# Optimization experiments

Measured on AMD Instinct MI355X. Metric: run time of the kernel, lower is better.

Reference implementation:

```python
import jax, jax.numpy as jnp
import numpy as np

N_NODES = 50000
N_EDGES = 640000
D_IN = 128
D_H1 = 128
D_H2 = 128
N_CLASSES = 64


def setup_inputs() -> dict:
    key = jax.random.key(0)
    ks = jax.random.split(key, 8)
    x = jax.random.normal(ks[0], (N_NODES, D_IN), dtype=jnp.float32)
    edge_index = jax.random.randint(ks[1], (2, N_EDGES), 0, N_NODES, dtype=jnp.int64)
    s1 = 1.0 / np.sqrt(D_IN)
    s2 = 1.0 / np.sqrt(D_H1)
    s3 = 1.0 / np.sqrt(D_H2)
    W1 = jax.random.uniform(ks[2], (D_IN, D_H1), jnp.float32, -s1, s1)
    b1 = jnp.zeros((D_H1,), jnp.float32)
    W2 = jax.random.uniform(ks[3], (D_H1, D_H2), jnp.float32, -s2, s2)
    b2 = jnp.zeros((D_H2,), jnp.float32)
    Wl = jax.random.uniform(ks[4], (D_H2, N_CLASSES), jnp.float32, -s3, s3)
    bl = jax.random.uniform(ks[5], (N_CLASSES,), jnp.float32, -s3, s3)
    return {"x": x, "edge_index": edge_index, "W1": W1, "b1": b1,
            "W2": W2, "b2": b2, "Wl": Wl, "bl": bl}


def _gcn_norm(edge_index, num_nodes):
    # PyG GCNConv: add self-loops, symmetric normalization D^-1/2 (A+I) D^-1/2
    loop = jnp.arange(num_nodes, dtype=edge_index.dtype)
    src = jnp.concatenate([edge_index[0], loop])
    dst = jnp.concatenate([edge_index[1], loop])
    deg = jax.ops.segment_sum(jnp.ones_like(dst, dtype=jnp.float32), dst,
                              num_segments=num_nodes)
    dinv = jnp.where(deg > 0, jax.lax.rsqrt(deg), 0.0)
    norm = dinv[src] * dinv[dst]  # [E+N]
    return src, dst, norm


def _gcn_conv(h, src, dst, norm, W, b, num_nodes):
    h = h @ W                       # transform first (smaller gather when D_out small)
    msg = h[src] * norm[:, None]    # gather + per-edge scale  [E+N, D_out]
    agg = jax.ops.segment_sum(msg, dst, num_segments=num_nodes)  # scatter-add
    return agg + b


def reference(x, edge_index, W1, b1, W2, b2, Wl, bl):
    n = x.shape[0]
    src, dst, norm = _gcn_norm(edge_index, n)
    h = jax.nn.relu(_gcn_conv(x, src, dst, norm, W1, b1, n))
    # dropout is identity in eval mode
    h = jax.nn.relu(_gcn_conv(h, src, dst, norm, W2, b2, n))
    return h @ Wl + bl
```

## Files before the change

kernel.cpp:

```cpp
#include <hip/hip_runtime.h>


typedef __attribute__((ext_vector_type(8))) __bf16 bf16x8;
typedef __attribute__((ext_vector_type(8))) short short8;
typedef __attribute__((ext_vector_type(4))) float f32x4;

__device__ inline float bf_lo(unsigned u) { return __uint_as_float(u << 16); }
__device__ inline float bf_hi(unsigned u) { return __uint_as_float(u & 0xffff0000u); }
__device__ inline unsigned short f2bf(float v) {
  return __builtin_bit_cast(unsigned short, (__bf16)v);
}

__global__ void k_count(const int* __restrict__ dst, int E, int* __restrict__ cnt) {
  int i = blockIdx.x * blockDim.x + threadIdx.x;
  if (i < E) atomicAdd(&cnt[dst[i]], 1);
}

__global__ void k_scan1(const int* __restrict__ cnt, int n, int* __restrict__ partial) {
  __shared__ int s[256];
  int i = blockIdx.x * 256 + threadIdx.x;
  s[threadIdx.x] = (i < n) ? cnt[i] : 0;
  __syncthreads();
  for (int off = 128; off > 0; off >>= 1) {
    if (threadIdx.x < off) s[threadIdx.x] += s[threadIdx.x + off];
    __syncthreads();
  }
  if (threadIdx.x == 0) partial[blockIdx.x] = s[0];
}

__global__ void k_scan2(int* __restrict__ partial, int nb) {
  __shared__ int s[256];
  int t = threadIdx.x;
  int v = (t < nb) ? partial[t] : 0;
  s[t] = v;
  __syncthreads();
  for (int off = 1; off < 256; off <<= 1) {
    int u = (t >= off) ? s[t - off] : 0;
    __syncthreads();
    s[t] += u;
    __syncthreads();
  }
  if (t < nb) partial[t] = s[t] - v;
}

__global__ void k_scan3(const int* __restrict__ cnt, const int* __restrict__ partial,
                        int n, int* __restrict__ row_off, int* __restrict__ cursor,
                        float* __restrict__ dinv) {
  __shared__ int s[256];
  int t = threadIdx.x;
  int i = blockIdx.x * 256 + t;
  int v = (i < n) ? cnt[i] : 0;
  s[t] = v;
  __syncthreads();
  for (int off = 1; off < 256; off <<= 1) {
    int u = (t >= off) ? s[t - off] : 0;
    __syncthreads();
    s[t] += u;
    __syncthreads();
  }
  int incl = s[t];
  int excl = incl - v;
  int base = partial[blockIdx.x];
  if (i < n) {
    row_off[i] = base + excl;
    cursor[i] = base + excl;
    dinv[i] = rsqrtf((float)(v + 1));
    if (i == n - 1) row_off[n] = base + incl;
  }
}

__global__ void k_place(const int* __restrict__ src, const int* __restrict__ dst, int E,
                        int* __restrict__ cursor, const float* __restrict__ dinv,
                        int2* __restrict__ edges) {
  int e = blockIdx.x * blockDim.x + threadIdx.x;
  if (e < E) {
    int s = src[e], d = dst[e];
    int pos = atomicAdd(&cursor[d], 1);
    edges[pos] = make_int2(s, __float_as_int(dinv[s] * dinv[d]));
  }
}

__global__ void k_prepW(const float* __restrict__ W1, const float* __restrict__ W2,
                        const float* __restrict__ Wl,
                        unsigned short* __restrict__ b1h, unsigned short* __restrict__ b1l,
                        unsigned short* __restrict__ b2h, unsigned short* __restrict__ b2l,
                        unsigned short* __restrict__ blh, unsigned short* __restrict__ bll) {
  int idx = blockIdx.x * 256 + threadIdx.x;
  const float* W;
  unsigned short *bh, *bl_;
  int N, local;
  if (idx < 16384)      { W = W1; bh = b1h; bl_ = b1l; N = 128; local = idx; }
  else if (idx < 32768) { W = W2; bh = b2h; bl_ = b2l; N = 128; local = idx - 16384; }
  else if (idx < 40960) { W = Wl; bh = blh; bl_ = bll; N = 64;  local = idx - 32768; }
  else return;
  int n = local >> 7, k = local & 127;
  float v = W[(size_t)k * N + n];
  __bf16 h = (__bf16)v;
  bh[local] = __builtin_bit_cast(unsigned short, h);
  bl_[local] = f2bf(v - (float)h);
}

__global__ __launch_bounds__(256) void k_prepX(const float* __restrict__ x,
                                               unsigned short* __restrict__ xh,
                                               unsigned short* __restrict__ xl, int total4) {
  int i = blockIdx.x * 256 + threadIdx.x;
  if (i >= total4) return;
  float4 v = ((const float4*)x)[i];
  ushort4 h, l;
  __bf16 h0 = (__bf16)v.x; h.x = __builtin_bit_cast(unsigned short, h0); l.x = f2bf(v.x - (float)h0);
  __bf16 h1 = (__bf16)v.y; h.y = __builtin_bit_cast(unsigned short, h1); l.y = f2bf(v.y - (float)h1);
  __bf16 h2 = (__bf16)v.z; h.z = __builtin_bit_cast(unsigned short, h2); l.z = f2bf(v.z - (float)h2);
  __bf16 h3 = (__bf16)v.w; h.w = __builtin_bit_cast(unsigned short, h3); l.w = f2bf(v.w - (float)h3);
  ((ushort4*)xh)[i] = h;
  ((ushort4*)xl)[i] = l;
}

template <int NT, bool BIAS, bool OUT_BF16>
__global__ __launch_bounds__(256) void gemm2(
    const unsigned short* __restrict__ Ahi, const unsigned short* __restrict__ Alo,
    const unsigned short* __restrict__ Bhi, const unsigned short* __restrict__ Blo,
    const float* __restrict__ bias, void* __restrict__ Cout, int M) {
  constexpr int K = 128;
  constexpr int NCOL = NT * 16;
  __shared__ alignas(16) unsigned short lbh[NCOL * K];
  __shared__ alignas(16) unsigned short lbl[NCOL * K];
  int t = threadIdx.x;
  for (int c = t; c < NCOL * 16; c += 256) {
    int r = c >> 4, q = c & 15;
    int sq = q ^ (r & 15);
    *(short8*)&lbh[r * K + sq * 8] = *(const short8*)&Bhi[r * K + q * 8];
    *(short8*)&lbl[r * K + sq * 8] = *(const short8*)&Blo[r * K + q * 8];
  }
  __syncthreads();

  int lane = t & 63, wave = t >> 6;
  int lm = lane & 15, lk = lane >> 4;
  int m_base = blockIdx.x * 128 + wave * 32;

  f32x4 acc[2][NT] = {};
  const short8 zero8 = {0, 0, 0, 0, 0, 0, 0, 0};

#pragma unroll
  for (int ks = 0; ks < 4; ++ks) {
    int k0 = ks * 32 + lk * 8;
    int chunk = (ks * 4 + lk);
    bf16x8 bh[NT], bl[NT];
#pragma unroll
    for (int nt = 0; nt < NT; ++nt) {
      int r = nt * 16 + lm;
      int sq = chunk ^ lm;
      bh[nt] = *(const bf16x8*)&lbh[r * K + sq * 8];
      bl[nt] = *(const bf16x8*)&lbl[r * K + sq * 8];
    }
#pragma unroll
    for (int mt = 0; mt < 2; ++mt) {
      int row = m_base + mt * 16 + lm;
      bf16x8 ah, al;
      if (row < M) {
        ah = *(const bf16x8*)&Ahi[(size_t)row * K + k0];
        al = *(const bf16x8*)&Alo[(size_t)row * K + k0];
      } else {
        ah = __builtin_bit_cast(bf16x8, zero8);
        al = __builtin_bit_cast(bf16x8, zero8);
      }
#pragma unroll
      for (int nt = 0; nt < NT; ++nt) {
        acc[mt][nt] = __builtin_amdgcn_mfma_f32_16x16x32_bf16(ah, bh[nt], acc[mt][nt], 0, 0, 0);
        acc[mt][nt] = __builtin_amdgcn_mfma_f32_16x16x32_bf16(ah, bl[nt], acc[mt][nt], 0, 0, 0);
        acc[mt][nt] = __builtin_amdgcn_mfma_f32_16x16x32_bf16(al, bh[nt], acc[mt][nt], 0, 0, 0);
      }
    }
  }

#pragma unroll
  for (int mt = 0; mt < 2; ++mt) {
#pragma unroll
    for (int r = 0; r < 4; ++r) {
      int row = m_base + mt * 16 + lk * 4 + r;
      if (row < M) {
#pragma unroll
        for (int nt = 0; nt < NT; ++nt) {
          int col = nt * 16 + lm;
          float v = acc[mt][nt][r];
          if (BIAS) v += bias[col];
          if (OUT_BF16)
            ((unsigned short*)Cout)[(size_t)row * NCOL + col] = f2bf(v);
          else
            ((float*)Cout)[(size_t)row * NCOL + col] = v;
        }
      }
    }
  }
}

__global__ __launch_bounds__(256) void k_agg(const unsigned short* __restrict__ t,
                      const int* __restrict__ row_off,
                      const int2* __restrict__ edges,
                      const float* __restrict__ dinv, const float* __restrict__ bias,
                      unsigned short* __restrict__ ghi, unsigned short* __restrict__ glo,
                      int n) {
  int wave = threadIdx.x >> 6;
  int lane = threadIdx.x & 63;
  int node = blockIdx.x * 4 + wave;
  if (node >= n) return;
  float di = dinv[node];
  float self = di * di;
  unsigned sv = *(const unsigned*)&t[(size_t)node * 128 + lane * 2];
  float ax = self * bf_lo(sv), ay = self * bf_hi(sv);
  float bx = 0.f, by = 0.f, cx = 0.f, cy = 0.f, dx = 0.f, dy = 0.f;
  int e0 = row_off[node], e1 = row_off[node + 1];
  int e = e0;
  for (; e + 4 <= e1; e += 4) {
    int2 p0 = edges[e], p1 = edges[e + 1], p2 = edges[e + 2], p3 = edges[e + 3];
    float w0 = __int_as_float(p0.y), w1 = __int_as_float(p1.y);
    float w2 = __int_as_float(p2.y), w3 = __int_as_float(p3.y);
    unsigned u0 = *(const unsigned*)&t[(size_t)p0.x * 128 + lane * 2];
    unsigned u1 = *(const unsigned*)&t[(size_t)p1.x * 128 + lane * 2];
    unsigned u2 = *(const unsigned*)&t[(size_t)p2.x * 128 + lane * 2];
    unsigned u3 = *(const unsigned*)&t[(size_t)p3.x * 128 + lane * 2];
    ax += w0 * bf_lo(u0); ay += w0 * bf_hi(u0);
    bx += w1 * bf_lo(u1); by += w1 * bf_hi(u1);
    cx += w2 * bf_lo(u2); cy += w2 * bf_hi(u2);
    dx += w3 * bf_lo(u3); dy += w3 * bf_hi(u3);
  }
  for (; e < e1; ++e) {
    int2 p = edges[e];
    float w = __int_as_float(p.y);
    unsigned u = *(const unsigned*)&t[(size_t)p.x * 128 + lane * 2];
    ax += w * bf_lo(u); ay += w * bf_hi(u);
  }
  float sx = (ax + bx) + (cx + dx);
  float sy = (ay + by) + (cy + dy);
  float2 bb = ((const float2*)bias)[lane];
  sx = fmaxf(sx + bb.x, 0.f);
  sy = fmaxf(sy + bb.y, 0.f);
  __bf16 hx = (__bf16)sx; float hxf = (float)hx;
  __bf16 hy = (__bf16)sy; float hyf = (float)hy;
  ushort2 ho, lo;
  ho.x = __builtin_bit_cast(unsigned short, hx);
  ho.y = __builtin_bit_cast(unsigned short, hy);
  lo.x = f2bf(sx - hxf);
  lo.y = f2bf(sy - hyf);
  *(ushort2*)&ghi[(size_t)node * 128 + lane * 2] = ho;
  *(ushort2*)&glo[(size_t)node * 128 + lane * 2] = lo;
}

extern "C" void kernel_launch(void* const* d_in, const int* in_sizes, int n_in,
                              void* d_out, int out_size, void* d_ws, size_t ws_size,
                              hipStream_t stream) {
  const float* x  = (const float*)d_in[0];
  const int*   ei = (const int*)d_in[1];
  const float* W1 = (const float*)d_in[2];
  const float* b1 = (const float*)d_in[3];
  const float* W2 = (const float*)d_in[4];
  const float* b2 = (const float*)d_in[5];
  const float* Wl = (const float*)d_in[6];
  const float* bl = (const float*)d_in[7];
  float* out = (float*)d_out;

  const int D = 128;
  int N = in_sizes[0] / D;
  int E = in_sizes[1] / 2;
  const int* src = ei;
  const int* dst = ei + E;

  uintptr_t ws = (uintptr_t)d_ws;
  auto take = [&](size_t bytes) {
    uintptr_t p = ws;
    ws += (bytes + 15) & ~(size_t)15;
    return p;
  };
  unsigned short* t_bf = (unsigned short*)take((size_t)N * D * 2);
  unsigned short* xh   = (unsigned short*)take((size_t)N * D * 2);
  unsigned short* xl   = (unsigned short*)take((size_t)N * D * 2);
  int2*  edges   = (int2*)take((size_t)E * 8);
  int*   cnt     = (int*)take((size_t)N * sizeof(int));
  int*   row_off = (int*)take(((size_t)N + 1) * sizeof(int));
  int*   cursor  = (int*)take((size_t)N * sizeof(int));
  float* dinv    = (float*)take((size_t)N * sizeof(float));
  int*   partial = (int*)take(256 * sizeof(int));
  unsigned short* b1h = (unsigned short*)take(128 * 128 * 2);
  unsigned short* b1l = (unsigned short*)take(128 * 128 * 2);
  unsigned short* b2h = (unsigned short*)take(128 * 128 * 2);
  unsigned short* b2l = (unsigned short*)take(128 * 128 * 2);
  unsigned short* blh = (unsigned short*)take(128 * 64 * 2);
  unsigned short* bll = (unsigned short*)take(128 * 64 * 2);

  int nb_n = (N + 255) / 256;
  int nb_e = (E + 255) / 256;

  hipMemsetAsync(cnt, 0, (size_t)N * sizeof(int), stream);
  k_count<<<nb_e, 256, 0, stream>>>(dst, E, cnt);
  k_scan1<<<nb_n, 256, 0, stream>>>(cnt, N, partial);
  k_scan2<<<1, 256, 0, stream>>>(partial, nb_n);
  k_scan3<<<nb_n, 256, 0, stream>>>(cnt, partial, N, row_off, cursor, dinv);
  k_place<<<nb_e, 256, 0, stream>>>(src, dst, E, cursor, dinv, edges);

  k_prepW<<<(40960 + 255) / 256, 256, 0, stream>>>(W1, W2, Wl, b1h, b1l, b2h, b2l, blh, bll);
  int total4 = N * D / 4;
  k_prepX<<<(total4 + 255) / 256, 256, 0, stream>>>(x, xh, xl, total4);

  int gemm_blocks = (N + 127) / 128;
  int agg_blocks = (N + 3) / 4;

  gemm2<8, false, true><<<gemm_blocks, 256, 0, stream>>>(xh, xl, b1h, b1l, nullptr, t_bf, N);
  k_agg<<<agg_blocks, 256, 0, stream>>>(t_bf, row_off, edges, dinv, b1, xh, xl, N);
  gemm2<8, false, true><<<gemm_blocks, 256, 0, stream>>>(xh, xl, b2h, b2l, nullptr, t_bf, N);
  k_agg<<<agg_blocks, 256, 0, stream>>>(t_bf, row_off, edges, dinv, b2, xh, xl, N);
  gemm2<4, true, false><<<gemm_blocks, 256, 0, stream>>>(xh, xl, blh, bll, bl, out, N);
}
```

Baseline: 268.8 us.

## Fuse x bf16 split into GEMM, merge scan passes, split-wave aggregation

The separate k_prepX pass is removed. The first GEMM now reads fp32 x directly and splits it into hi/lo bf16 in registers, which saves a full write and re-read of the split x arrays. The scan2 kernel is folded into scan3: each block reduces the preceding partial sums itself, dropping one launch at the cost of redundant reductions. The aggregation kernel now has the two half-waves each take alternate edges with 8-byte feature loads and combine results via shuffle. The edge placement uses a packed 64-bit nontemporal store.

```diff
diff --git a/kernel.cpp b/kernel.cpp
--- a/kernel.cpp
+++ b/kernel.cpp
@@ -28,10 +28,25 @@
   if (threadIdx.x == 0) partial[blockIdx.x] = s[0];
 }
 
-__global__ void k_scan2(int* __restrict__ partial, int nb) {
+__global__ void k_scan3(const int* __restrict__ cnt, const int* __restrict__ partial,
+                        int nb, int n, int* __restrict__ row_off, int* __restrict__ cursor,
+                        float* __restrict__ dinv) {
   __shared__ int s[256];
+  __shared__ int base_s;
   int t = threadIdx.x;
-  int v = (t < nb) ? partial[t] : 0;
+  s[t] = (t < nb && t < (int)blockIdx.x) ? partial[t] : 0;
+  __syncthreads();
+  for (int off = 128; off > 0; off >>= 1) {
+    if (t < off) s[t] += s[t + off];
+    __syncthreads();
+  }
+  if (t == 0) base_s = s[0];
+  __syncthreads();
+  int base = base_s;
+  __syncthreads();
+
+  int i = blockIdx.x * 256 + t;
+  int v = (i < n) ? cnt[i] : 0;
   s[t] = v;
   __syncthreads();
   for (int off = 1; off < 256; off <<= 1) {
@@ -40,27 +55,8 @@
     s[t] += u;
     __syncthreads();
   }
-  if (t < nb) partial[t] = s[t] - v;
-}
-
-__global__ void k_scan3(const int* __restrict__ cnt, const int* __restrict__ partial,
-                        int n, int* __restrict__ row_off, int* __restrict__ cursor,
-                        float* __restrict__ dinv) {
-  __shared__ int s[256];
-  int t = threadIdx.x;
-  int i = blockIdx.x * 256 + t;
-  int v = (i < n) ? cnt[i] : 0;
-  s[t] = v;
-  __syncthreads();
-  for (int off = 1; off < 256; off <<= 1) {
-    int u = (t >= off) ? s[t - off] : 0;
-    __syncthreads();
-    s[t] += u;
-    __syncthreads();
-  }
   int incl = s[t];
   int excl = incl - v;
-  int base = partial[blockIdx.x];
   if (i < n) {
     row_off[i] = base + excl;
     cursor[i] = base + excl;
@@ -71,12 +67,15 @@
 
 __global__ void k_place(const int* __restrict__ src, const int* __restrict__ dst, int E,
                         int* __restrict__ cursor, const float* __restrict__ dinv,
-                        int2* __restrict__ edges) {
+                        unsigned long long* __restrict__ edges) {
   int e = blockIdx.x * blockDim.x + threadIdx.x;
   if (e < E) {
     int s = src[e], d = dst[e];
     int pos = atomicAdd(&cursor[d], 1);
-    edges[pos] = make_int2(s, __float_as_int(dinv[s] * dinv[d]));
+    unsigned long long packed =
+        (unsigned long long)(unsigned)s |
+        ((unsigned long long)__float_as_uint(dinv[s] * dinv[d]) << 32);
+    __builtin_nontemporal_store(packed, &edges[pos]);
   }
 }
 
@@ -100,24 +99,9 @@
   bl_[local] = f2bf(v - (float)h);
 }
 
-__global__ __launch_bounds__(256) void k_prepX(const float* __restrict__ x,
-                                               unsigned short* __restrict__ xh,
-                                               unsigned short* __restrict__ xl, int total4) {
-  int i = blockIdx.x * 256 + threadIdx.x;
-  if (i >= total4) return;
-  float4 v = ((const float4*)x)[i];
-  ushort4 h, l;
-  __bf16 h0 = (__bf16)v.x; h.x = __builtin_bit_cast(unsigned short, h0); l.x = f2bf(v.x - (float)h0);
-  __bf16 h1 = (__bf16)v.y; h.y = __builtin_bit_cast(unsigned short, h1); l.y = f2bf(v.y - (float)h1);
-  __bf16 h2 = (__bf16)v.z; h.z = __builtin_bit_cast(unsigned short, h2); l.z = f2bf(v.z - (float)h2);
-  __bf16 h3 = (__bf16)v.w; h.w = __builtin_bit_cast(unsigned short, h3); l.w = f2bf(v.w - (float)h3);
-  ((ushort4*)xh)[i] = h;
-  ((ushort4*)xl)[i] = l;
-}
-
-template <int NT, bool BIAS, bool OUT_BF16>
+template <int NT, bool A32, bool BIAS, bool OUT_BF16>
 __global__ __launch_bounds__(256) void gemm2(
-    const unsigned short* __restrict__ Ahi, const unsigned short* __restrict__ Alo,
+    const void* __restrict__ Ahi_, const unsigned short* __restrict__ Alo,
     const unsigned short* __restrict__ Bhi, const unsigned short* __restrict__ Blo,
     const float* __restrict__ bias, void* __restrict__ Cout, int M) {
   constexpr int K = 128;
@@ -156,12 +140,31 @@
     for (int mt = 0; mt < 2; ++mt) {
       int row = m_base + mt * 16 + lm;
       bf16x8 ah, al;
-      if (row < M) {
-        ah = *(const bf16x8*)&Ahi[(size_t)row * K + k0];
-        al = *(const bf16x8*)&Alo[(size_t)row * K + k0];
+      if (A32) {
+        const float* Af = (const float*)Ahi_;
+        if (row < M) {
+          float4 v0 = *(const float4*)&Af[(size_t)row * K + k0];
+          float4 v1 = *(const float4*)&Af[(size_t)row * K + k0 + 4];
+          float a[8] = {v0.x, v0.y, v0.z, v0.w, v1.x, v1.y, v1.z, v1.w};
+#pragma unroll
+          for (int j = 0; j < 8; ++j) {
+            __bf16 h = (__bf16)a[j];
+            ah[j] = h;
+            al[j] = (__bf16)(a[j] - (float)h);
+          }
+        } else {
+          ah = __builtin_bit_cast(bf16x8, zero8);
+          al = __builtin_bit_cast(bf16x8, zero8);
+        }
       } else {
-        ah = __builtin_bit_cast(bf16x8, zero8);
-        al = __builtin_bit_cast(bf16x8, zero8);
+        const unsigned short* Ahi = (const unsigned short*)Ahi_;
+        if (row < M) {
+          ah = *(const bf16x8*)&Ahi[(size_t)row * K + k0];
+          al = *(const bf16x8*)&Alo[(size_t)row * K + k0];
+        } else {
+          ah = __builtin_bit_cast(bf16x8, zero8);
+          al = __builtin_bit_cast(bf16x8, zero8);
+        }
       }
 #pragma unroll
       for (int nt = 0; nt < NT; ++nt) {
@@ -201,48 +204,69 @@
                       int n) {
   int wave = threadIdx.x >> 6;
   int lane = threadIdx.x & 63;
+  int half = lane >> 5;
+  int hl = lane & 31;
   int node = blockIdx.x * 4 + wave;
   if (node >= n) return;
-  float di = dinv[node];
-  float self = di * di;
-  unsigned sv = *(const unsigned*)&t[(size_t)node * 128 + lane * 2];
-  float ax = self * bf_lo(sv), ay = self * bf_hi(sv);
-  float bx = 0.f, by = 0.f, cx = 0.f, cy = 0.f, dx = 0.f, dy = 0.f;
   int e0 = row_off[node], e1 = row_off[node + 1];
-  int e = e0;
-  for (; e + 4 <= e1; e += 4) {
-    int2 p0 = edges[e], p1 = edges[e + 1], p2 = edges[e + 2], p3 = edges[e + 3];
+
+  float4 a0 = {0,0,0,0}, a1 = {0,0,0,0}, a2 = {0,0,0,0}, a3 = {0,0,0,0};
+  int e = e0 + half;
+  for (; e + 6 < e1; e += 8) {
+    int2 p0 = edges[e],     p1 = edges[e + 2];
+    int2 p2 = edges[e + 4], p3 = edges[e + 6];
+    uint2 u0 = *(const uint2*)&t[(size_t)p0.x * 128 + hl * 4];
+    uint2 u1 = *(const uint2*)&t[(size_t)p1.x * 128 + hl * 4];
+    uint2 u2 = *(const uint2*)&t[(size_t)p2.x * 128 + hl * 4];
+    uint2 u3 = *(const uint2*)&t[(size_t)p3.x * 128 + hl * 4];
     float w0 = __int_as_float(p0.y), w1 = __int_as_float(p1.y);
     float w2 = __int_as_float(p2.y), w3 = __int_as_float(p3.y);
-    unsigned u0 = *(const unsigned*)&t[(size_t)p0.x * 128 + lane * 2];
-    unsigned u1 = *(const unsigned*)&t[(size_t)p1.x * 128 + lane * 2];
-    unsigned u2 = *(const unsigned*)&t[(size_t)p2.x * 128 + lane * 2];
-    unsigned u3 = *(const unsigned*)&t[(size_t)p3.x * 128 + lane * 2];
-    ax += w0 * bf_lo(u0); ay += w0 * bf_hi(u0);
-    bx += w1 * bf_lo(u1); by += w1 * bf_hi(u1);
-    cx += w2 * bf_lo(u2); cy += w2 * bf_hi(u2);
-    dx += w3 * bf_lo(u3); dy += w3 * bf_hi(u3);
-  }
-  for (; e < e1; ++e) {
+    a0.x += w0 * bf_lo(u0.x); a0.y += w0 * bf_hi(u0.x);
+    a0.z += w0 * bf_lo(u0.y); a0.w += w0 * bf_hi(u0.y);
+    a1.x += w1 * bf_lo(u1.x); a1.y += w1 * bf_hi(u1.x);
+    a1.z += w1 * bf_lo(u1.y); a1.w += w1 * bf_hi(u1.y);
+    a2.x += w2 * bf_lo(u2.x); a2.y += w2 * bf_hi(u2.x);
+    a2.z += w2 * bf_lo(u2.y); a2.w += w2 * bf_hi(u2.y);
+    a3.x += w3 * bf_lo(u3.x); a3.y += w3 * bf_hi(u3.x);
+    a3.z += w3 * bf_lo(u3.y); a3.w += w3 * bf_hi(u3.y);
+  }
+  for (; e < e1; e += 2) {
     int2 p = edges[e];
+    uint2 u = *(const uint2*)&t[(size_t)p.x * 128 + hl * 4];
     float w = __int_as_float(p.y);
-    unsigned u = *(const unsigned*)&t[(size_t)p.x * 128 + lane * 2];
-    ax += w * bf_lo(u); ay += w * bf_hi(u);
-  }
-  float sx = (ax + bx) + (cx + dx);
-  float sy = (ay + by) + (cy + dy);
-  float2 bb = ((const float2*)bias)[lane];
-  sx = fmaxf(sx + bb.x, 0.f);
-  sy = fmaxf(sy + bb.y, 0.f);
-  __bf16 hx = (__bf16)sx; float hxf = (float)hx;
-  __bf16 hy = (__bf16)sy; float hyf = (float)hy;
-  ushort2 ho, lo;
-  ho.x = __builtin_bit_cast(unsigned short, hx);
-  ho.y = __builtin_bit_cast(unsigned short, hy);
-  lo.x = f2bf(sx - hxf);
-  lo.y = f2bf(sy - hyf);
-  *(ushort2*)&ghi[(size_t)node * 128 + lane * 2] = ho;
-  *(ushort2*)&glo[(size_t)node * 128 + lane * 2] = lo;
+    a0.x += w * bf_lo(u.x); a0.y += w * bf_hi(u.x);
+    a0.z += w * bf_lo(u.y); a0.w += w * bf_hi(u.y);
+  }
+  float sx = (a0.x + a1.x) + (a2.x + a3.x);
+  float sy = (a0.y + a1.y) + (a2.y + a3.y);
+  float sz = (a0.z + a1.z) + (a2.z + a3.z);
+  float sw = (a0.w + a1.w) + (a2.w + a3.w);
+  sx += __shfl_xor(sx, 32);
+  sy += __shfl_xor(sy, 32);
+  sz += __shfl_xor(sz, 32);
+  sw += __shfl_xor(sw, 32);
+  if (half == 0) {
+    float di = dinv[node];
+    float self = di * di;
+    uint2 sv = *(const uint2*)&t[(size_t)node * 128 + hl * 4];
+    sx += self * bf_lo(sv.x); sy += self * bf_hi(sv.x);
+    sz += self * bf_lo(sv.y); sw += self * bf_hi(sv.y);
+    float4 bb = *(const float4*)&bias[hl * 4];
+    sx = fmaxf(sx + bb.x, 0.f); sy = fmaxf(sy + bb.y, 0.f);
+    sz = fmaxf(sz + bb.z, 0.f); sw = fmaxf(sw + bb.w, 0.f);
+    __bf16 hx = (__bf16)sx, hy = (__bf16)sy, hz = (__bf16)sz, hw = (__bf16)sw;
+    ushort4 ho, lo;
+    ho.x = __builtin_bit_cast(unsigned short, hx);
+    ho.y = __builtin_bit_cast(unsigned short, hy);
+    ho.z = __builtin_bit_cast(unsigned short, hz);
+    ho.w = __builtin_bit_cast(unsigned short, hw);
+    lo.x = f2bf(sx - (float)hx);
+    lo.y = f2bf(sy - (float)hy);
+    lo.z = f2bf(sz - (float)hz);
+    lo.w = f2bf(sw - (float)hw);
+    *(ushort4*)&ghi[(size_t)node * 128 + hl * 4] = ho;
+    *(ushort4*)&glo[(size_t)node * 128 + hl * 4] = lo;
+  }
 }
 
 extern "C" void kernel_launch(void* const* d_in, const int* in_sizes, int n_in,
@@ -273,7 +297,7 @@
   unsigned short* t_bf = (unsigned short*)take((size_t)N * D * 2);
   unsigned short* xh   = (unsigned short*)take((size_t)N * D * 2);
   unsigned short* xl   = (unsigned short*)take((size_t)N * D * 2);
-  int2*  edges   = (int2*)take((size_t)E * 8);
+  unsigned long long* edges = (unsigned long long*)take((size_t)E * 8);
   int*   cnt     = (int*)take((size_t)N * sizeof(int));
   int*   row_off = (int*)take(((size_t)N + 1) * sizeof(int));
   int*   cursor  = (int*)take((size_t)N * sizeof(int));
@@ -292,20 +316,17 @@
   hipMemsetAsync(cnt, 0, (size_t)N * sizeof(int), stream);
   k_count<<<nb_e, 256, 0, stream>>>(dst, E, cnt);
   k_scan1<<<nb_n, 256, 0, stream>>>(cnt, N, partial);
-  k_scan2<<<1, 256, 0, stream>>>(partial, nb_n);
-  k_scan3<<<nb_n, 256, 0, stream>>>(cnt, partial, N, row_off, cursor, dinv);
+  k_scan3<<<nb_n, 256, 0, stream>>>(cnt, partial, nb_n, N, row_off, cursor, dinv);
   k_place<<<nb_e, 256, 0, stream>>>(src, dst, E, cursor, dinv, edges);
 
   k_prepW<<<(40960 + 255) / 256, 256, 0, stream>>>(W1, W2, Wl, b1h, b1l, b2h, b2l, blh, bll);
-  int total4 = N * D / 4;
-  k_prepX<<<(total4 + 255) / 256, 256, 0, stream>>>(x, xh, xl, total4);
 
   int gemm_blocks = (N + 127) / 128;
   int agg_blocks = (N + 3) / 4;
 
-  gemm2<8, false, true><<<gemm_blocks, 256, 0, stream>>>(xh, xl, b1h, b1l, nullptr, t_bf, N);
-  k_agg<<<agg_blocks, 256, 0, stream>>>(t_bf, row_off, edges, dinv, b1, xh, xl, N);
-  gemm2<8, false, true><<<gemm_blocks, 256, 0, stream>>>(xh, xl, b2h, b2l, nullptr, t_bf, N);
-  k_agg<<<agg_blocks, 256, 0, stream>>>(t_bf, row_off, edges, dinv, b2, xh, xl, N);
-  gemm2<4, true, false><<<gemm_blocks, 256, 0, stream>>>(xh, xl, blh, bll, bl, out, N);
-}
+  gemm2<8, true, false, true><<<gemm_blocks, 256, 0, stream>>>(x, nullptr, b1h, b1l, nullptr, t_bf, N);
+  k_agg<<<agg_blocks, 256, 0, stream>>>(t_bf, row_off, (const int2*)edges, dinv, b1, xh, xl, N);
+  gemm2<8, false, false, true><<<gemm_blocks, 256, 0, stream>>>(xh, xl, b2h, b2l, nullptr, t_bf, N);
+  k_agg<<<agg_blocks, 256, 0, stream>>>(t_bf, row_off, (const int2*)edges, dinv, b2, xh, xl, N);
+  gemm2<4, false, true, false><<<gemm_blocks, 256, 0, stream>>>(xh, xl, blh, bll, bl, out, N);
+}
```

Result: faster. 260.6 us (-3.0%).
